# Kernel optimization log

Measured on AMD Instinct MI355X. Metric: run time of the kernel, lower is better.

Reference implementation:

```python
import jax, jax.numpy as jnp
import numpy as np

B, S, HID = 2, 2048, 4096
NH, NKV, D = 32, 8, 128
GROUPS = NH // NKV


def _rotate_half(x):
    x1, x2 = jnp.split(x, 2, axis=-1)
    return jnp.concatenate((-x2, x1), axis=-1)


def setup_inputs() -> dict:
    key = jax.random.key(0)
    ks = jax.random.split(key, 5)
    hidden_states = jax.random.normal(ks[0], (B, S, HID), jnp.float32)
    Wq = jax.random.normal(ks[1], (HID, NH * D), jnp.float32) * (1.0 / np.float32(np.sqrt(HID)))
    Wk = jax.random.normal(ks[2], (HID, NKV * D), jnp.float32) * (1.0 / np.float32(np.sqrt(HID)))
    Wv = jax.random.normal(ks[3], (HID, NKV * D), jnp.float32) * (1.0 / np.float32(np.sqrt(HID)))
    Wo = jax.random.normal(ks[4], (NH * D, HID), jnp.float32) * (1.0 / np.float32(np.sqrt(NH * D)))
    # RoPE caches (Llama-style, base 10000)
    inv_freq = (1.0 / (10000.0 ** (np.arange(0, D, 2, dtype=np.float32) / D))).astype(np.float32)
    t = np.arange(S, dtype=np.float32)
    freqs = np.outer(t, inv_freq)  # [S, D/2]
    emb = np.concatenate([freqs, freqs], axis=-1)  # [S, D]
    cos_cache = jnp.asarray(np.cos(emb), jnp.float32)
    sin_cache = jnp.asarray(np.sin(emb), jnp.float32)
    position_ids = jnp.broadcast_to(jnp.arange(S, dtype=jnp.int64), (B, S))
    # causal mask used by scaled_qk's torch.where (True = attend)
    causal = jnp.tril(jnp.ones((S, S), dtype=bool))
    attention_mask = jnp.broadcast_to(causal[None, None], (B, 1, S, S))
    return {
        "hidden_states": hidden_states, "Wq": Wq, "Wk": Wk, "Wv": Wv, "Wo": Wo,
        "cos_cache": cos_cache, "sin_cache": sin_cache,
        "position_ids": position_ids, "attention_mask": attention_mask,
    }


def reference(hidden_states, Wq, Wk, Wv, Wo, cos_cache, sin_cache, position_ids, attention_mask):
    b, s, _ = hidden_states.shape
    # qkv_proj + move_heads_front -> [b, heads, s, d]
    Q = (hidden_states @ Wq).reshape(b, s, NH, D).transpose(0, 2, 1, 3)
    K = (hidden_states @ Wk).reshape(b, s, NKV, D).transpose(0, 2, 1, 3)
    V = (hidden_states @ Wv).reshape(b, s, NKV, D).transpose(0, 2, 1, 3)
    # RoPE
    cos = cos_cache[position_ids][:, None]  # [b,1,s,d]
    sin = sin_cache[position_ids][:, None]
    Q = Q * cos + _rotate_half(Q) * sin
    K = K * cos + _rotate_half(K) * sin
    # repeat_kv
    K = jnp.repeat(K, GROUPS, axis=1)  # [b,NH,s,d]
    V = jnp.repeat(V, GROUPS, axis=1)
    # scaled QK + mask + softmax (fp32) + PV
    scores = jnp.einsum("bhsd,bhtd->bhst", Q, K) / np.float32(np.sqrt(D))
    scores = jnp.where(attention_mask, scores, jnp.finfo(scores.dtype).min)
    probs = jax.nn.softmax(scores.astype(jnp.float32), axis=-1).astype(Q.dtype)
    attn = jnp.einsum("bhst,bhtd->bhsd", probs, V)
    # o_proj
    out = attn.transpose(0, 2, 1, 3).reshape(b, s, NH * D) @ Wo
    return out
```

## Files before the change

### kernel.cpp

```cpp
#include <hip/hip_runtime.h>

#define B_ 2
#define S_ 2048
#define HID_ 4096
#define NH_ 32
#define NKV_ 8
#define D_ 128
#define M_ (B_*S_)
#define NQKV_ (HID_ + 2*NKV_*D_)

typedef __bf16 v8bf __attribute__((ext_vector_type(8)));
typedef float  v4f  __attribute__((ext_vector_type(4)));
typedef float  v16f __attribute__((ext_vector_type(16)));

__device__ __forceinline__ unsigned short f2bf(float x) {
    unsigned u = __float_as_uint(x);
    u += 0x7FFFu + ((u >> 16) & 1u);
    return (unsigned short)(u >> 16);
}
__device__ __forceinline__ float bf2f(unsigned short h) {
    return __uint_as_float(((unsigned)h) << 16);
}
__device__ __forceinline__ unsigned pack2bf(float a, float b) {
    return (unsigned)f2bf(a) | ((unsigned)f2bf(b) << 16);
}
__device__ __forceinline__ float exp2g(float x) {
    return __builtin_amdgcn_exp2f(x);
}

__device__ __forceinline__ void gl_lds16(const unsigned short* g, unsigned short* l) {
    __builtin_amdgcn_global_load_lds(
        (const __attribute__((address_space(1))) void*)g,
        (__attribute__((address_space(3))) void*)l, 16, 0, 0);
}

__global__ __launch_bounds__(256)
void cvt_f32_bf16(const float* __restrict__ src, unsigned short* __restrict__ dst, int n4) {
    int i = blockIdx.x * 256 + threadIdx.x;
    if (i >= n4) return;
    float4 v = ((const float4*)src)[i];
    ushort4 o;
    o.x = f2bf(v.x); o.y = f2bf(v.y); o.z = f2bf(v.z); o.w = f2bf(v.w);
    ((ushort4*)dst)[i] = o;
}

__global__ __launch_bounds__(256)
void transpose_f32_bf16(const float* __restrict__ src,
                        unsigned short* __restrict__ dst, int K, int N) {
    __shared__ unsigned short tile[64][65];
    int n0 = blockIdx.x * 64, k0 = blockIdx.y * 64;
    int tid = threadIdx.x;
    for (int i = 0; i < 16; ++i) {
        int fi = tid + i * 256;
        int r = fi >> 6, c = fi & 63;
        tile[r][c] = f2bf(src[(size_t)(k0 + r) * N + n0 + c]);
    }
    __syncthreads();
    for (int i = 0; i < 16; ++i) {
        int fi = tid + i * 256;
        int r = fi >> 6, c = fi & 63;
        dst[(size_t)(n0 + r) * K + k0 + c] = tile[c][r];
    }
}

__global__ __launch_bounds__(256)
void transpose_v(const unsigned short* __restrict__ src,
                 unsigned short* __restrict__ dst) {
    __shared__ unsigned short tile[64][65];
    int s0 = blockIdx.x * 64, d0 = blockIdx.y * 64;
    size_t base = (size_t)blockIdx.z * S_ * D_;
    int tid = threadIdx.x;
    for (int i = 0; i < 16; ++i) {
        int fi = tid + i * 256;
        int r = fi >> 6, c = fi & 63;
        tile[r][c] = src[base + (size_t)(s0 + r) * D_ + d0 + c];
    }
    __syncthreads();
    for (int i = 0; i < 16; ++i) {
        int fi = tid + i * 256;
        int r = fi >> 6, c = fi & 63;
        dst[base + (size_t)(d0 + r) * S_ + s0 + c] = tile[c][r];
    }
}

template <int MODE>
__global__ __launch_bounds__(256)
void gemm_bt(const unsigned short* __restrict__ A,
             const unsigned short* __restrict__ BT,
             int K, int lda, int ldb,
             unsigned short* __restrict__ outQ,
             unsigned short* __restrict__ outK,
             unsigned short* __restrict__ outV,
             float* __restrict__ outF) {
    __shared__ unsigned short As[128][32];
    __shared__ unsigned short Bs[128][32];
    int tid = threadIdx.x;
    int lane = tid & 63, wid = tid >> 6;
    int quad = lane >> 4, l16 = lane & 15;
    int wr = wid >> 1, wc = wid & 1;
    int r0 = blockIdx.y * 128, n0 = blockIdx.x * 128;

    v4f zero = {0.f, 0.f, 0.f, 0.f};
    v4f acc[4][4];
    for (int i = 0; i < 4; ++i) for (int j = 0; j < 4; ++j) acc[i][j] = zero;

    const int srow = wid * 32 + (lane >> 2);
    const int sch  = (lane & 3) * 8;
    const unsigned short* gA = &A [(size_t)(r0 + srow) * lda + sch];
    const unsigned short* gB = &BT[(size_t)(n0 + srow) * ldb + sch];
    unsigned short* lA0 = &As[wid * 32][0];
    unsigned short* lA1 = &As[wid * 32 + 16][0];
    unsigned short* lB0 = &Bs[wid * 32][0];
    unsigned short* lB1 = &Bs[wid * 32 + 16][0];

    for (int kt = 0; kt < K / 32; ++kt) {
        int kk = kt * 32;
        gl_lds16(gA + kk, lA0);
        gl_lds16(gA + (size_t)16 * lda + kk, lA1);
        gl_lds16(gB + kk, lB0);
        gl_lds16(gB + (size_t)16 * ldb + kk, lB1);
        __syncthreads();
        v8bf av[4], bv[4];
        for (int ms = 0; ms < 4; ++ms) av[ms] = *(const v8bf*)&As[wr * 64 + ms * 16 + l16][quad * 8];
        for (int ns = 0; ns < 4; ++ns) bv[ns] = *(const v8bf*)&Bs[wc * 64 + ns * 16 + l16][quad * 8];
        for (int ms = 0; ms < 4; ++ms)
            for (int ns = 0; ns < 4; ++ns)
                acc[ms][ns] = __builtin_amdgcn_mfma_f32_16x16x32_bf16(av[ms], bv[ns], acc[ms][ns], 0, 0, 0);
        __syncthreads();
    }

    for (int ms = 0; ms < 4; ++ms)
        for (int ns = 0; ns < 4; ++ns)
            for (int r = 0; r < 4; ++r) {
                int row = r0 + wr * 64 + ms * 16 + quad * 4 + r;
                int col = n0 + wc * 64 + ns * 16 + l16;
                if (MODE == 1) {
                    outF[(size_t)row * HID_ + col] = acc[ms][ns][r];
                } else {
                    unsigned short hv = f2bf(acc[ms][ns][r]);
                    int b = row >> 11, s = row & (S_ - 1);
                    if (col < HID_) {
                        int h = col >> 7, d = col & 127;
                        outQ[((size_t)((b * NH_ + h) * S_ + s)) * D_ + d] = hv;
                    } else if (col < HID_ + NKV_ * D_) {
                        int j = col - HID_; int h = j >> 7, d = j & 127;
                        outK[((size_t)((b * NKV_ + h) * S_ + s)) * D_ + d] = hv;
                    } else {
                        int j = col - HID_ - NKV_ * D_; int h = j >> 7, d = j & 127;
                        outV[((size_t)((b * NKV_ + h) * S_ + s)) * D_ + d] = hv;
                    }
                }
            }
}

__global__ __launch_bounds__(256)
void rope_kernel(unsigned short* __restrict__ buf,
                 const float* __restrict__ cosc,
                 const float* __restrict__ sinc, int total) {
    int idx = blockIdx.x * 256 + threadIdx.x;
    if (idx >= total) return;
    int d2 = idx & 63;
    int s  = (idx >> 6) & (S_ - 1);
    int bh = idx >> 17;
    size_t base = ((size_t)bh * S_ + s) * D_;
    float c  = cosc[s * D_ + d2];
    float sn = sinc[s * D_ + d2];
    float x1 = bf2f(buf[base + d2]);
    float x2 = bf2f(buf[base + d2 + 64]);
    buf[base + d2]      = f2bf(x1 * c - x2 * sn);
    buf[base + d2 + 64] = f2bf(x2 * c + x1 * sn);
}

__global__ __launch_bounds__(256)
void flash_attn(const unsigned short* __restrict__ Q,
                const unsigned short* __restrict__ Kb,
                const unsigned short* __restrict__ VT,
                unsigned short* __restrict__ O) {
    __shared__ unsigned short Ks[64 * 128];
    __shared__ unsigned short Vt[128 * 64];
    int tid = threadIdx.x;
    int lane = tid & 63, w = tid >> 6;
    int l31 = lane & 31, hi = lane >> 5;
    int p = blockIdx.x;
    int h = blockIdx.y, b = blockIdx.z;

    const int hkv = h >> 2;
    const size_t kvbase = (size_t)(b * NKV_ + hkv) * S_ * D_;
    const size_t vtbase = kvbase;

    int krow[4], kch[4], vrow[4], vch[4];
    #pragma unroll
    for (int i = 0; i < 4; ++i) {
        int idx = tid + i * 256;
        krow[i] = idx >> 4; kch[i] = idx & 15;
        vrow[i] = idx >> 3; vch[i] = idx & 7;
    }
    const int vsw = (l31 & 7) << 3;

    for (int ph = 0; ph < 2; ++ph) {
        const int qt = ph == 0 ? 15 - p : p;
        const int qbase = qt * 128 + w * 32;

        const size_t qoff = ((size_t)(b * NH_ + h) * S_ + qbase + l31) * D_ + hi * 8;
        v8bf aq[8];
        #pragma unroll
        for (int kt = 0; kt < 8; ++kt) aq[kt] = *(const v8bf*)&Q[qoff + kt * 16];

        v16f o[4];
        #pragma unroll
        for (int n = 0; n < 4; ++n)
            #pragma unroll
            for (int r = 0; r < 16; ++r) o[n][r] = 0.f;
        float m2 = -1e30f, l_ = 0.f;

        const int ntB = 2 * qt + 2;
        const int twmax = (qbase + 31) >> 6;

        uint4 kpre[4], vpre[4];
        #pragma unroll
        for (int i = 0; i < 4; ++i) {
            kpre[i] = *(const uint4*)&Kb[kvbase + (size_t)krow[i] * D_ + kch[i] * 8];
            vpre[i] = *(const uint4*)&VT[vtbase + (size_t)vrow[i] * S_ + vch[i] * 8];
        }

        for (int t = 0; t < ntB; ++t) {
            int kv0 = t * 64;
            __syncthreads();
            #pragma unroll
            for (int i = 0; i < 4; ++i) {
                *(uint4*)&Ks[(size_t)krow[i] * 128 + ((kch[i] * 8) ^ ((krow[i] & 7) << 3))] = kpre[i];
                *(uint4*)&Vt[(size_t)vrow[i] * 64 + ((vch[i] * 8) ^ ((vrow[i] & 7) << 3))] = vpre[i];
            }
            __syncthreads();
            if (t + 1 < ntB) {
                int nkv0 = kv0 + 64;
                #pragma unroll
                for (int i = 0; i < 4; ++i) {
                    kpre[i] = *(const uint4*)&Kb[kvbase + (size_t)(nkv0 + krow[i]) * D_ + kch[i] * 8];
                    vpre[i] = *(const uint4*)&VT[vtbase + (size_t)vrow[i] * S_ + nkv0 + vch[i] * 8];
                }
            }
            if (t > twmax) continue;

            v16f s0, s1;
            #pragma unroll
            for (int r = 0; r < 16; ++r) { s0[r] = 0.f; s1[r] = 0.f; }
            #pragma unroll
            for (int kt = 0; kt < 8; ++kt) {
                int cw = (kt * 16 + hi * 8) ^ ((l31 & 7) << 3);
                v8bf k0 = *(const v8bf*)&Ks[(size_t)l31 * 128 + cw];
                v8bf k1 = *(const v8bf*)&Ks[(size_t)(32 + l31) * 128 + cw];
                s0 = __builtin_amdgcn_mfma_f32_32x32x16_bf16(k0, aq[kt], s0, 0, 0, 0);
                s1 = __builtin_amdgcn_mfma_f32_32x32x16_bf16(k1, aq[kt], s1, 0, 0, 0);
            }

            if (kv0 + 63 > qbase) {
                int vq = qbase + l31 - kv0 - 4 * hi;
                #pragma unroll
                for (int r = 0; r < 16; ++r) {
                    int c0 = (r & 3) + 8 * (r >> 2);
                    if (c0 > vq)      s0[r] = -1e30f;
                    if (c0 + 32 > vq) s1[r] = -1e30f;
                }
            }
            float rm = fmaxf(s0[0], s1[0]);
            #pragma unroll
            for (int r = 1; r < 16; ++r) rm = fmaxf(rm, fmaxf(s0[r], s1[r]));
            rm = fmaxf(rm, __shfl_xor(rm, 32));
            const float cexp = 0.1275279431f;
            float m2n = fmaxf(m2, rm * cexp);
            float al = exp2g(m2 - m2n);
            float rs = 0.f;
            #pragma unroll
            for (int r = 0; r < 16; ++r) {
                s0[r] = exp2g(__builtin_fmaf(s0[r], cexp, -m2n));
                s1[r] = exp2g(__builtin_fmaf(s1[r], cexp, -m2n));
                rs += s0[r] + s1[r];
            }
            rs += __shfl_xor(rs, 32);
            l_ = l_ * al + rs;
            m2 = m2n;
            #pragma unroll
            for (int n = 0; n < 4; ++n)
                #pragma unroll
                for (int r = 0; r < 16; ++r) o[n][r] *= al;

            unsigned pk0[4][2], pk1[4][2];
            #pragma unroll
            for (int g = 0; g < 4; ++g) {
                pk0[g][0] = pack2bf(s0[4*g],   s0[4*g+1]);
                pk0[g][1] = pack2bf(s0[4*g+2], s0[4*g+3]);
                pk1[g][0] = pack2bf(s1[4*g],   s1[4*g+1]);
                pk1[g][1] = pack2bf(s1[4*g+2], s1[4*g+3]);
            }
            const bool hb = (hi != 0);
            #pragma unroll
            for (int kb = 0; kb < 4; ++kb) {
                const int g0 = (kb & 1) * 2;
                unsigned la, lb, oa, ob;
                if (kb < 2) { la = pk0[g0][0]; lb = pk0[g0][1]; oa = pk0[g0+1][0]; ob = pk0[g0+1][1]; }
                else        { la = pk1[g0][0]; lb = pk1[g0][1]; oa = pk1[g0+1][0]; ob = pk1[g0+1][1]; }
                unsigned sa0 = hb ? la : oa, sa1 = hb ? lb : ob;
                unsigned ra0 = (unsigned)__shfl_xor((int)sa0, 32);
                unsigned ra1 = (unsigned)__shfl_xor((int)sa1, 32);
                unsigned ma0 = hb ? oa : la, ma1 = hb ? ob : lb;
                union { unsigned u[4]; v8bf v; } pf;
                pf.u[0] = hb ? ra0 : ma0; pf.u[1] = hb ? ra1 : ma1;
                pf.u[2] = hb ? ma0 : ra0; pf.u[3] = hb ? ma1 : ra1;
                #pragma unroll
                for (int n = 0; n < 4; ++n) {
                    v8bf av = *(const v8bf*)&Vt[(size_t)(n * 32 + l31) * 64 + ((kb * 16 + hi * 8) ^ vsw)];
                    o[n] = __builtin_amdgcn_mfma_f32_32x32x16_bf16(av, pf.v, o[n], 0, 0, 0);
                }
            }
        }

        float inv = 1.0f / l_;
        int q = qbase + l31;
        size_t obase = ((size_t)(b * S_ + q)) * HID_ + h * D_;
        #pragma unroll
        for (int n = 0; n < 4; ++n)
            #pragma unroll
            for (int rg = 0; rg < 4; ++rg) {
                ushort4 st;
                st.x = f2bf(o[n][4*rg+0] * inv);
                st.y = f2bf(o[n][4*rg+1] * inv);
                st.z = f2bf(o[n][4*rg+2] * inv);
                st.w = f2bf(o[n][4*rg+3] * inv);
                *(ushort4*)&O[obase + n * 32 + 8 * rg + 4 * hi] = st;
            }
    }
}

extern "C" void kernel_launch(void* const* d_in, const int* in_sizes, int n_in,
                              void* d_out, int out_size, void* d_ws, size_t ws_size,
                              hipStream_t stream) {
    const float* hid  = (const float*)d_in[0];
    const float* Wq   = (const float*)d_in[1];
    const float* Wk   = (const float*)d_in[2];
    const float* Wv   = (const float*)d_in[3];
    const float* Wo   = (const float*)d_in[4];
    const float* cosc = (const float*)d_in[5];
    const float* sinc = (const float*)d_in[6];

    unsigned short* ws    = (unsigned short*)d_ws;
    unsigned short* wqkvT = ws;
    unsigned short* qbuf  = ws + (size_t)NQKV_ * HID_;
    unsigned short* kbuf  = qbuf + (size_t)B_ * NH_ * S_ * D_;
    unsigned short* vbuf  = kbuf + (size_t)B_ * NKV_ * S_ * D_;
    unsigned short* hidB  = vbuf + (size_t)B_ * NKV_ * S_ * D_;
    unsigned short* attn  = ws;
    unsigned short* woT   = ws + (size_t)M_ * HID_;
    unsigned short* vTbuf = hidB;

    cvt_f32_bf16<<<(M_ * HID_ / 4 + 255) / 256, 256, 0, stream>>>(hid, hidB, M_ * HID_ / 4);
    transpose_f32_bf16<<<dim3(64, 64), 256, 0, stream>>>(Wq, wqkvT, HID_, HID_);
    transpose_f32_bf16<<<dim3(16, 64), 256, 0, stream>>>(Wk, wqkvT + (size_t)HID_ * HID_, HID_, NKV_ * D_);
    transpose_f32_bf16<<<dim3(16, 64), 256, 0, stream>>>(Wv, wqkvT + (size_t)(HID_ + NKV_ * D_) * HID_, HID_, NKV_ * D_);
    gemm_bt<0><<<dim3(NQKV_ / 128, M_ / 128), 256, 0, stream>>>(
        hidB, wqkvT, HID_, HID_, HID_, qbuf, kbuf, vbuf, nullptr);
    rope_kernel<<<(B_ * NH_ * S_ * 64) / 256, 256, 0, stream>>>(qbuf, cosc, sinc, B_ * NH_ * S_ * 64);
    rope_kernel<<<(B_ * NKV_ * S_ * 64) / 256, 256, 0, stream>>>(kbuf, cosc, sinc, B_ * NKV_ * S_ * 64);
    transpose_v<<<dim3(S_ / 64, D_ / 64, B_ * NKV_), 256, 0, stream>>>(vbuf, vTbuf);
    flash_attn<<<dim3(8, NH_, B_), 256, 0, stream>>>(qbuf, kbuf, vTbuf, attn);
    transpose_f32_bf16<<<dim3(64, 64), 256, 0, stream>>>(Wo, woT, HID_, HID_);
    gemm_bt<1><<<dim3(HID_ / 128, M_ / 128), 256, 0, stream>>>(
        attn, woT, HID_, HID_, HID_, nullptr, nullptr, nullptr, (float*)d_out);
}
```

Baseline: 1.070 ms.

## Add lazy softmax rescaling, MFMA priority hints, and native bf16 conversion in attention

The online softmax now rescales the output accumulators and running sum only when some lane's new max exceeds the stored max by a threshold. Otherwise it keeps the stale max, which avoids 64 multiplies per tile and an exp on most iterations. MFMA blocks are wrapped in s_setprio to raise wave priority during matrix work, and the manual round-to-nearest bf16 conversion is replaced by the compiler's native __bf16 cast. The lazy rescale lets exponentials grow up to 2^11.5 before renormalising, which may affect accuracy of the bf16-packed probabilities.

```diff
diff --git a/kernel.cpp b/kernel.cpp
--- a/kernel.cpp
+++ b/kernel.cpp
@@ -21,8 +21,12 @@
 __device__ __forceinline__ float bf2f(unsigned short h) {
     return __uint_as_float(((unsigned)h) << 16);
 }
+__device__ __forceinline__ unsigned short bfbits(float x) {
+    __bf16 b = (__bf16)x;
+    return __builtin_bit_cast(unsigned short, b);
+}
 __device__ __forceinline__ unsigned pack2bf(float a, float b) {
-    return (unsigned)f2bf(a) | ((unsigned)f2bf(b) << 16);
+    return (unsigned)bfbits(a) | ((unsigned)bfbits(b) << 16);
 }
 __device__ __forceinline__ float exp2g(float x) {
     return __builtin_amdgcn_exp2f(x);
@@ -245,6 +249,7 @@
             v16f s0, s1;
             #pragma unroll
             for (int r = 0; r < 16; ++r) { s0[r] = 0.f; s1[r] = 0.f; }
+            __builtin_amdgcn_s_setprio(1);
             #pragma unroll
             for (int kt = 0; kt < 8; ++kt) {
                 int cw = (kt * 16 + hi * 8) ^ ((l31 & 7) << 3);
@@ -253,6 +258,7 @@
                 s0 = __builtin_amdgcn_mfma_f32_32x32x16_bf16(k0, aq[kt], s0, 0, 0, 0);
                 s1 = __builtin_amdgcn_mfma_f32_32x32x16_bf16(k1, aq[kt], s1, 0, 0, 0);
             }
+            __builtin_amdgcn_s_setprio(0);
 
             if (kv0 + 63 > qbase) {
                 int vq = qbase + l31 - kv0 - 4 * hi;
@@ -265,25 +271,29 @@
             }
             float rm = fmaxf(s0[0], s1[0]);
             #pragma unroll
-            for (int r = 1; r < 16; ++r) rm = fmaxf(rm, fmaxf(s0[r], s1[r]));
+            for (int r = 1; r < 16; ++r) rm = fmaxf(fmaxf(rm, s0[r]), s1[r]);
             rm = fmaxf(rm, __shfl_xor(rm, 32));
             const float cexp = 0.1275279431f;
-            float m2n = fmaxf(m2, rm * cexp);
-            float al = exp2g(m2 - m2n);
+            float d = rm * cexp - m2;
+            if (__any(d > 11.5416f)) {
+                float m2n = fmaxf(m2, rm * cexp);
+                float al = exp2g(m2 - m2n);
+                l_ *= al;
+                #pragma unroll
+                for (int n = 0; n < 4; ++n)
+                    #pragma unroll
+                    for (int r = 0; r < 16; ++r) o[n][r] *= al;
+                m2 = m2n;
+            }
             float rs = 0.f;
             #pragma unroll
             for (int r = 0; r < 16; ++r) {
-                s0[r] = exp2g(__builtin_fmaf(s0[r], cexp, -m2n));
-                s1[r] = exp2g(__builtin_fmaf(s1[r], cexp, -m2n));
+                s0[r] = exp2g(__builtin_fmaf(s0[r], cexp, -m2));
+                s1[r] = exp2g(__builtin_fmaf(s1[r], cexp, -m2));
                 rs += s0[r] + s1[r];
             }
             rs += __shfl_xor(rs, 32);
-            l_ = l_ * al + rs;
-            m2 = m2n;
-            #pragma unroll
-            for (int n = 0; n < 4; ++n)
-                #pragma unroll
-                for (int r = 0; r < 16; ++r) o[n][r] *= al;
+            l_ += rs;
 
             unsigned pk0[4][2], pk1[4][2];
             #pragma unroll
@@ -307,11 +317,13 @@
                 union { unsigned u[4]; v8bf v; } pf;
                 pf.u[0] = hb ? ra0 : ma0; pf.u[1] = hb ? ra1 : ma1;
                 pf.u[2] = hb ? ma0 : ra0; pf.u[3] = hb ? ma1 : ra1;
+                __builtin_amdgcn_s_setprio(1);
                 #pragma unroll
                 for (int n = 0; n < 4; ++n) {
                     v8bf av = *(const v8bf*)&Vt[(size_t)(n * 32 + l31) * 64 + ((kb * 16 + hi * 8) ^ vsw)];
                     o[n] = __builtin_amdgcn_mfma_f32_32x32x16_bf16(av, pf.v, o[n], 0, 0, 0);
                 }
+                __builtin_amdgcn_s_setprio(0);
             }
         }
 
@@ -323,10 +335,10 @@
             #pragma unroll
             for (int rg = 0; rg < 4; ++rg) {
                 ushort4 st;
-                st.x = f2bf(o[n][4*rg+0] * inv);
-                st.y = f2bf(o[n][4*rg+1] * inv);
-                st.z = f2bf(o[n][4*rg+2] * inv);
-                st.w = f2bf(o[n][4*rg+3] * inv);
+                st.x = bfbits(o[n][4*rg+0] * inv);
+                st.y = bfbits(o[n][4*rg+1] * inv);
+                st.z = bfbits(o[n][4*rg+2] * inv);
+                st.w = bfbits(o[n][4*rg+3] * inv);
                 *(ushort4*)&O[obase + n * 32 + 8 * rg + 4 * hi] = st;
             }
     }
```

Measured after the change: 1.065 ms. About the same (-0.5%).
